# Optimization experiments

Hardware: AMD Instinct MI355X
Metric: run time of the kernel (lower is better)

## Reference

```python
import jax, jax.numpy as jnp
import numpy as np

FFT_LENGTH = 2048
HOP_LENGTH = 512  # window_length // 4, window_length == fft_length


def _hann_periodic(n):
    # tf.signal.hann_window(n, periodic=True)
    return (0.5 - 0.5 * jnp.cos(2.0 * jnp.pi * jnp.arange(n) / n)).astype(jnp.float32)


def setup_inputs() -> dict:
    key = jax.random.key(0)
    k1, k2 = jax.random.split(key)
    B, F, NB = 4, 4000, FFT_LENGTH // 2 + 1
    spec_real = jax.random.normal(k1, (B, F, NB), dtype=jnp.float32)
    spec_imag = jax.random.normal(k2, (B, F, NB), dtype=jnp.float32)
    return {"spec_real": spec_real, "spec_imag": spec_imag}


def reference(spec_real, spec_imag) -> jnp.ndarray:
    fft_length, hop = FFT_LENGTH, HOP_LENGTH
    B, F, _ = spec_real.shape
    window = _hann_periodic(fft_length)  # [N], window_length == fft_length so no padding

    # irfft of the complex spectrogram -> time-domain frames [B, F, N]
    frames = jnp.fft.irfft(spec_real + 1j * spec_imag, n=fft_length).astype(jnp.float32)
    windowed = window * frames  # [B, F, N]

    # overlap-and-add: output length L = (F-1)*hop + N
    L = (F - 1) * hop + fft_length
    idx = (jnp.arange(F) * hop)[:, None] + jnp.arange(fft_length)[None, :]  # [F, N]
    out = jnp.zeros((B, L), jnp.float32).at[:, idx].add(windowed)

    # librosa window_sumsquare: overlap-add of squared window, guard tiny values
    wsq = jnp.zeros((L,), jnp.float32).at[idx].add(window * window)
    tiny = jnp.float32(np.finfo(np.float32).tiny)
    window_sum = jnp.where(wsq > tiny, wsq, jnp.float32(1.0))

    y = out / window_sum
    # center=True: trim fft_length//2 on each side
    half = fft_length // 2
    return y[:, half:L - half]
```

## Files before the change

kernel.cpp:

```cpp
#include <hip/hip_runtime.h>
#include <math.h>

#define NB       1025
#define M        1024
#define FFTN     2048
#define HOP      512
#define NFRAMES  4000
#define BATCH    4
#define OUT_T    2047488
#define R_HOPS   8
#define REG_PB   501
#define PI_F     3.14159265358979323846f

__device__ __forceinline__ float2 cmul(float2 a, float2 b) {
    return make_float2(a.x*b.x - a.y*b.y, a.x*b.y + a.y*b.x);
}
__device__ __forceinline__ int SW(int i) { return i ^ ((i >> 4) & 15); }

__device__ __forceinline__ float wsq_at(int p) {
    int u  = p + FFTN / 2;
    int fm = u >> 9;
    int n0 = u & 511;
    float wsq = 0.f;
    #pragma unroll
    for (int jj = 0; jj < 4; ++jj) {
        int fr = fm - jj;
        if (fr >= 0 && fr < NFRAMES) {
            int n = n0 + (jj << 9);
            float sw = __sinf((PI_F / (float)FFTN) * (float)n);
            float w  = sw * sw;
            wsq += w * w;
        }
    }
    const float tiny = 1.17549435e-38f;
    return (wsq > tiny) ? wsq : 1.0f;
}

__device__ __forceinline__ float invw_at(int p, bool edge) {
    if (edge && (p < 512 || p >= OUT_T - 512)) return 1.0f / wsq_at(p);
    return (2.0f / 3.0f);
}

template<int ST>
__device__ __forceinline__ void stage(const float2* __restrict__ src,
                                      float2* __restrict__ dst, int j, float2 w1) {
    const int Ns = 1 << (2 * ST);
    float2 v0 = src[SW(j)];
    float2 v1 = src[SW(j + 256)];
    float2 v2 = src[SW(j + 512)];
    float2 v3 = src[SW(j + 768)];
    float2 w2 = cmul(w1, w1);
    float2 w3 = cmul(w2, w1);
    v1 = cmul(v1, w1); v2 = cmul(v2, w2); v3 = cmul(v3, w3);
    float2 t0 = make_float2(v0.x + v2.x, v0.y + v2.y);
    float2 t1 = make_float2(v0.x - v2.x, v0.y - v2.y);
    float2 t2 = make_float2(v1.x + v3.x, v1.y + v3.y);
    float2 t3 = make_float2(v1.x - v3.x, v1.y - v3.y);
    int jm = j & (Ns - 1);
    int idxD = ((j >> (2 * ST)) << (2 * ST + 2)) + jm;
    dst[SW(idxD         )] = make_float2(t0.x + t2.x, t0.y + t2.y);
    dst[SW(idxD +     Ns)] = make_float2(t1.x - t3.y, t1.y + t3.x);
    dst[SW(idxD + 2 * Ns)] = make_float2(t0.x - t2.x, t0.y - t2.y);
    dst[SW(idxD + 3 * Ns)] = make_float2(t1.x + t3.y, t1.y - t3.x);
}

__device__ __forceinline__ void pack_st0(float2* __restrict__ dst, int j,
                                         const float2* tw_pack,
                                         const float* car, const float* cai,
                                         const float* cbr, const float* cbi) {
    float2 z[4];
    #pragma unroll
    for (int kk = 0; kk < 4; ++kk) {
        float arv = car[kk], aiv = cai[kk];
        float brv = cbr[kk], biv = cbi[kk];
        if (kk == 0 && j == 0) { aiv = 0.f; biv = 0.f; }
        float Er = 0.5f * (arv + brv), Ei = 0.5f * (aiv - biv);
        float Dr = 0.5f * (arv - brv), Di = 0.5f * (aiv + biv);
        float2 t = tw_pack[kk];
        float Or = Dr * t.x - Di * t.y;
        float Oi = Dr * t.y + Di * t.x;
        z[kk] = make_float2(Er - Oi, Ei + Or);
    }
    float2 t0 = make_float2(z[0].x + z[2].x, z[0].y + z[2].y);
    float2 t1 = make_float2(z[0].x - z[2].x, z[0].y - z[2].y);
    float2 t2 = make_float2(z[1].x + z[3].x, z[1].y + z[3].y);
    float2 t3 = make_float2(z[1].x - z[3].x, z[1].y - z[3].y);
    dst[SW(4*j    )] = make_float2(t0.x + t2.x, t0.y + t2.y);
    dst[SW(4*j + 1)] = make_float2(t1.x - t3.y, t1.y + t3.x);
    dst[SW(4*j + 2)] = make_float2(t0.x - t2.x, t0.y - t2.y);
    dst[SW(4*j + 3)] = make_float2(t1.x + t3.y, t1.y - t3.x);
}

__device__ __forceinline__ void load_spec(const float* __restrict__ sr,
                                          const float* __restrict__ si,
                                          int b, int f, int j,
                                          float* car, float* cai,
                                          float* cbr, float* cbi) {
    const size_t fb = ((size_t)b * NFRAMES + f) * NB;
    const float* __restrict__ xr = sr + fb;
    const float* __restrict__ xi = si + fb;
    #pragma unroll
    for (int kk = 0; kk < 4; ++kk) {
        int k  = j + kk * 256;
        int mk = M - k;
        car[kk] = xr[k];  cai[kk] = xi[k];
        cbr[kk] = xr[mk]; cbi[kk] = xi[mk];
    }
}

__global__ __launch_bounds__(256) void istft_regacc_kernel(
    const float* __restrict__ sr, const float* __restrict__ si,
    float* __restrict__ out)
{
    __shared__ float2 buf0[M];
    __shared__ float2 buf1[M];

    const int blk = blockIdx.x;
    const int b   = blk / REG_PB;
    const int reg = blk - b * REG_PB;
    const int s0h = reg * R_HOPS;
    const int j   = threadIdx.x;
    const bool edge = (reg == 0) || (reg == REG_PB - 1);

    float2 tw_pack[4];
    #pragma unroll
    for (int kk = 0; kk < 4; ++kk) {
        int k = j + kk * 256;
        float s, c;
        __sincosf(PI_F * (float)k * (1.0f / (float)M), &s, &c);
        tw_pack[kk] = make_float2(c, s);
    }
    float2 w1s[4];
    #pragma unroll
    for (int st = 1; st <= 4; ++st) {
        int Ns = 1 << (2 * st);
        int jm = j & (Ns - 1);
        float ang = (0.5f * PI_F / (float)Ns) * (float)jm;
        float s1, c1;
        __sincosf(ang, &s1, &c1);
        w1s[st-1] = make_float2(c1, s1);
    }
    float wreg[4][2];
    #pragma unroll
    for (int q = 0; q < 4; ++q) {
        int n = j + q * 256;
        #pragma unroll
        for (int h = 0; h < 2; ++h) {
            int t = 2 * n + h;
            float swv = __sinf((PI_F / (float)FFTN) * (float)t);
            wreg[q][h] = swv * swv * (1.0f / 1024.0f);
        }
    }

    float2 A[R_HOPS];
    #pragma unroll
    for (int s = 0; s < R_HOPS; ++s) A[s] = make_float2(0.f, 0.f);

    const int fbase = s0h - 3;

    float car[4], cai[4], cbr[4], cbi[4];
    {
        int it0 = (fbase < 0) ? -fbase : 0;
        int ff  = fbase + it0;
        if (ff > NFRAMES - 1) ff = NFRAMES - 1;
        load_spec(sr, si, b, ff, j, car, cai, cbr, cbi);
    }

    #pragma unroll
    for (int it = 0; it < 11; ++it) {
        const int f = fbase + it;
        const bool valid = (f >= 0) && (f < NFRAMES);
        if (valid) {
            pack_st0(buf0, j, tw_pack, car, cai, cbr, cbi);

            float nar[4], nai[4], nbr[4], nbi[4];
            const int fn = f + 1;
            const bool nvalid = (it < 10) && (fn < NFRAMES);
            if (nvalid) load_spec(sr, si, b, fn, j, nar, nai, nbr, nbi);

            __syncthreads();
            stage<1>(buf0, buf1, j, w1s[0]);
            __syncthreads();
            stage<2>(buf1, buf0, j, w1s[1]);
            __syncthreads();
            stage<3>(buf0, buf1, j, w1s[2]);
            __syncthreads();

            {
                float2 v0 = buf1[SW(j)];
                float2 v1 = buf1[SW(j + 256)];
                float2 v2 = buf1[SW(j + 512)];
                float2 v3 = buf1[SW(j + 768)];
                float2 w1 = w1s[3];
                float2 w2 = cmul(w1, w1);
                float2 w3 = cmul(w2, w1);
                v1 = cmul(v1, w1); v2 = cmul(v2, w2); v3 = cmul(v3, w3);
                float2 t0 = make_float2(v0.x + v2.x, v0.y + v2.y);
                float2 t1 = make_float2(v0.x - v2.x, v0.y - v2.y);
                float2 t2 = make_float2(v1.x + v3.x, v1.y + v3.y);
                float2 t3 = make_float2(v1.x - v3.x, v1.y - v3.y);
                float2 g[4];
                g[0] = make_float2(t0.x + t2.x, t0.y + t2.y);
                g[1] = make_float2(t1.x - t3.y, t1.y + t3.x);
                g[2] = make_float2(t0.x - t2.x, t0.y - t2.y);
                g[3] = make_float2(t1.x + t3.y, t1.y - t3.x);
                #pragma unroll
                for (int q = 0; q < 4; ++q) {
                    const int s = it - 3 + q;
                    if (s >= 0 && s < R_HOPS) {
                        A[s].x += g[q].x * wreg[q][0];
                        A[s].y += g[q].y * wreg[q][1];
                    }
                }
            }

            if (nvalid) {
                #pragma unroll
                for (int kk = 0; kk < 4; ++kk) {
                    car[kk] = nar[kk]; cai[kk] = nai[kk];
                    cbr[kk] = nbr[kk]; cbi[kk] = nbi[kk];
                }
            }
        }
    }

    const int base_u = s0h * HOP;
    float* outb = out + (size_t)b * OUT_T;
    #pragma unroll
    for (int s = 0; s < R_HOPS; ++s) {
        int i2 = j + 256 * s;
        int p0 = base_u + 2 * i2 - FFTN / 2;
        int p1 = p0 + 1;
        if ((unsigned)p0 < (unsigned)OUT_T) outb[p0] = A[s].x * invw_at(p0, edge);
        if ((unsigned)p1 < (unsigned)OUT_T) outb[p1] = A[s].y * invw_at(p1, edge);
    }
}

extern "C" void kernel_launch(void* const* d_in, const int* in_sizes, int n_in,
                              void* d_out, int out_size, void* d_ws, size_t ws_size,
                              hipStream_t stream) {
    const float* sr = (const float*)d_in[0];
    const float* si = (const float*)d_in[1];
    float* out = (float*)d_out;
    istft_regacc_kernel<<<BATCH * REG_PB, 256, 0, stream>>>(sr, si, out);
}
```

Baseline: 56.88 us.

## Process two overlap-add regions per block with float4-packed FFT stages

Each block now computes two adjacent output regions, running two frames' inverse FFTs at once by packing them into float4 shared-memory elements. This halves the block count and amortizes barriers and twiddle math across two transforms. The next-frame register prefetch is dropped, so loads are no longer overlapped with compute, and shared memory use and register pressure both double.

```diff
diff --git a/kernel.cpp b/kernel.cpp
--- a/kernel.cpp
+++ b/kernel.cpp
@@ -9,13 +9,22 @@
 #define BATCH    4
 #define OUT_T    2047488
 #define R_HOPS   8
-#define REG_PB   501
+#define NPAIR    251
 #define PI_F     3.14159265358979323846f
 
 __device__ __forceinline__ float2 cmul(float2 a, float2 b) {
     return make_float2(a.x*b.x - a.y*b.y, a.x*b.y + a.y*b.x);
 }
-__device__ __forceinline__ int SW(int i) { return i ^ ((i >> 4) & 15); }
+__device__ __forceinline__ float4 cmul4(float4 v, float2 w) {
+    return make_float4(v.x*w.x - v.y*w.y, v.x*w.y + v.y*w.x,
+                       v.z*w.x - v.w*w.y, v.z*w.y + v.w*w.x);
+}
+__device__ __forceinline__ float4 f4add(float4 a, float4 b){ return make_float4(a.x+b.x, a.y+b.y, a.z+b.z, a.w+b.w); }
+__device__ __forceinline__ float4 f4sub(float4 a, float4 b){ return make_float4(a.x-b.x, a.y-b.y, a.z-b.z, a.w-b.w); }
+__device__ __forceinline__ float4 f4addi(float4 a, float4 b){ return make_float4(a.x-b.y, a.y+b.x, a.z-b.w, a.w+b.z); }
+__device__ __forceinline__ float4 f4subi(float4 a, float4 b){ return make_float4(a.x+b.y, a.y-b.x, a.z+b.w, a.w-b.z); }
+
+__device__ __forceinline__ int SW4(int i) { return i ^ ((i >> 3) & 7); }
 
 __device__ __forceinline__ float wsq_at(int p) {
     int u  = p + FFTN / 2;
@@ -35,60 +44,30 @@
     const float tiny = 1.17549435e-38f;
     return (wsq > tiny) ? wsq : 1.0f;
 }
-
 __device__ __forceinline__ float invw_at(int p, bool edge) {
     if (edge && (p < 512 || p >= OUT_T - 512)) return 1.0f / wsq_at(p);
     return (2.0f / 3.0f);
 }
 
 template<int ST>
-__device__ __forceinline__ void stage(const float2* __restrict__ src,
-                                      float2* __restrict__ dst, int j, float2 w1) {
+__device__ __forceinline__ void stage4x(const float4* __restrict__ src,
+                                        float4* __restrict__ dst, int j, float2 w1) {
     const int Ns = 1 << (2 * ST);
-    float2 v0 = src[SW(j)];
-    float2 v1 = src[SW(j + 256)];
-    float2 v2 = src[SW(j + 512)];
-    float2 v3 = src[SW(j + 768)];
+    float4 v0 = src[SW4(j)];
+    float4 v1 = src[SW4(j + 256)];
+    float4 v2 = src[SW4(j + 512)];
+    float4 v3 = src[SW4(j + 768)];
     float2 w2 = cmul(w1, w1);
     float2 w3 = cmul(w2, w1);
-    v1 = cmul(v1, w1); v2 = cmul(v2, w2); v3 = cmul(v3, w3);
-    float2 t0 = make_float2(v0.x + v2.x, v0.y + v2.y);
-    float2 t1 = make_float2(v0.x - v2.x, v0.y - v2.y);
-    float2 t2 = make_float2(v1.x + v3.x, v1.y + v3.y);
-    float2 t3 = make_float2(v1.x - v3.x, v1.y - v3.y);
+    v1 = cmul4(v1, w1); v2 = cmul4(v2, w2); v3 = cmul4(v3, w3);
+    float4 t0 = f4add(v0, v2), t1 = f4sub(v0, v2);
+    float4 t2 = f4add(v1, v3), t3 = f4sub(v1, v3);
     int jm = j & (Ns - 1);
     int idxD = ((j >> (2 * ST)) << (2 * ST + 2)) + jm;
-    dst[SW(idxD         )] = make_float2(t0.x + t2.x, t0.y + t2.y);
-    dst[SW(idxD +     Ns)] = make_float2(t1.x - t3.y, t1.y + t3.x);
-    dst[SW(idxD + 2 * Ns)] = make_float2(t0.x - t2.x, t0.y - t2.y);
-    dst[SW(idxD + 3 * Ns)] = make_float2(t1.x + t3.y, t1.y - t3.x);
-}
-
-__device__ __forceinline__ void pack_st0(float2* __restrict__ dst, int j,
-                                         const float2* tw_pack,
-                                         const float* car, const float* cai,
-                                         const float* cbr, const float* cbi) {
-    float2 z[4];
-    #pragma unroll
-    for (int kk = 0; kk < 4; ++kk) {
-        float arv = car[kk], aiv = cai[kk];
-        float brv = cbr[kk], biv = cbi[kk];
-        if (kk == 0 && j == 0) { aiv = 0.f; biv = 0.f; }
-        float Er = 0.5f * (arv + brv), Ei = 0.5f * (aiv - biv);
-        float Dr = 0.5f * (arv - brv), Di = 0.5f * (aiv + biv);
-        float2 t = tw_pack[kk];
-        float Or = Dr * t.x - Di * t.y;
-        float Oi = Dr * t.y + Di * t.x;
-        z[kk] = make_float2(Er - Oi, Ei + Or);
-    }
-    float2 t0 = make_float2(z[0].x + z[2].x, z[0].y + z[2].y);
-    float2 t1 = make_float2(z[0].x - z[2].x, z[0].y - z[2].y);
-    float2 t2 = make_float2(z[1].x + z[3].x, z[1].y + z[3].y);
-    float2 t3 = make_float2(z[1].x - z[3].x, z[1].y - z[3].y);
-    dst[SW(4*j    )] = make_float2(t0.x + t2.x, t0.y + t2.y);
-    dst[SW(4*j + 1)] = make_float2(t1.x - t3.y, t1.y + t3.x);
-    dst[SW(4*j + 2)] = make_float2(t0.x - t2.x, t0.y - t2.y);
-    dst[SW(4*j + 3)] = make_float2(t1.x + t3.y, t1.y - t3.x);
+    dst[SW4(idxD         )] = f4add(t0, t2);
+    dst[SW4(idxD +     Ns)] = f4addi(t1, t3);
+    dst[SW4(idxD + 2 * Ns)] = f4sub(t0, t2);
+    dst[SW4(idxD + 3 * Ns)] = f4subi(t1, t3);
 }
 
 __device__ __forceinline__ void load_spec(const float* __restrict__ sr,
@@ -108,19 +87,49 @@
     }
 }
 
-__global__ __launch_bounds__(256) void istft_regacc_kernel(
+__device__ __forceinline__ void pack2_st0(float4* __restrict__ dst, int j,
+                                          const float2* twp,
+                                          const float* a1r, const float* a1i,
+                                          const float* b1r, const float* b1i,
+                                          const float* a2r, const float* a2i,
+                                          const float* b2r, const float* b2i) {
+    float4 z[4];
+    #pragma unroll
+    for (int kk = 0; kk < 4; ++kk) {
+        float ar = a1r[kk], ai = a1i[kk], br = b1r[kk], bi = b1i[kk];
+        float cr = a2r[kk], ci = a2i[kk], dr = b2r[kk], di = b2i[kk];
+        if (kk == 0 && j == 0) { ai = 0.f; bi = 0.f; ci = 0.f; di = 0.f; }
+        float2 t = twp[kk];
+        float Er = 0.5f*(ar+br), Ei = 0.5f*(ai-bi), Dr = 0.5f*(ar-br), Di = 0.5f*(ai+bi);
+        float Or = Dr*t.x - Di*t.y, Oi = Dr*t.y + Di*t.x;
+        float Fr = 0.5f*(cr+dr), Fi = 0.5f*(ci-di), Gr = 0.5f*(cr-dr), Gi = 0.5f*(ci+di);
+        float Pr = Gr*t.x - Gi*t.y, Pi = Gr*t.y + Gi*t.x;
+        z[kk] = make_float4(Er - Oi, Ei + Or, Fr - Pi, Fi + Pr);
+    }
+    float4 t0 = f4add(z[0], z[2]), t1 = f4sub(z[0], z[2]);
+    float4 t2 = f4add(z[1], z[3]), t3 = f4sub(z[1], z[3]);
+    dst[SW4(4*j    )] = f4add(t0, t2);
+    dst[SW4(4*j + 1)] = f4addi(t1, t3);
+    dst[SW4(4*j + 2)] = f4sub(t0, t2);
+    dst[SW4(4*j + 3)] = f4subi(t1, t3);
+}
+
+__global__ __launch_bounds__(256) void istft_pair_kernel(
     const float* __restrict__ sr, const float* __restrict__ si,
     float* __restrict__ out)
 {
-    __shared__ float2 buf0[M];
-    __shared__ float2 buf1[M];
-
-    const int blk = blockIdx.x;
-    const int b   = blk / REG_PB;
-    const int reg = blk - b * REG_PB;
-    const int s0h = reg * R_HOPS;
-    const int j   = threadIdx.x;
-    const bool edge = (reg == 0) || (reg == REG_PB - 1);
+    __shared__ float4 buf0[M];
+    __shared__ float4 buf1[M];
+
+    const int blk  = blockIdx.x;
+    const int b    = blk / NPAIR;
+    const int pr   = blk - b * NPAIR;
+    const int regA = 2 * pr;
+    const int s0hA = regA * R_HOPS;
+    const int s0hB = s0hA + R_HOPS;
+    const int j    = threadIdx.x;
+    const bool edgeA = (regA == 0) || (regA == 500);
+    const bool edgeB = (regA + 1 == 500);
 
     float2 tw_pack[4];
     #pragma unroll
@@ -152,87 +161,100 @@
         }
     }
 
-    float2 A[R_HOPS];
-    #pragma unroll
-    for (int s = 0; s < R_HOPS; ++s) A[s] = make_float2(0.f, 0.f);
-
-    const int fbase = s0h - 3;
-
-    float car[4], cai[4], cbr[4], cbi[4];
-    {
-        int it0 = (fbase < 0) ? -fbase : 0;
-        int ff  = fbase + it0;
-        if (ff > NFRAMES - 1) ff = NFRAMES - 1;
-        load_spec(sr, si, b, ff, j, car, cai, cbr, cbi);
+    float2 AccA[R_HOPS], AccB[R_HOPS];
+    #pragma unroll
+    for (int s = 0; s < R_HOPS; ++s) {
+        AccA[s] = make_float2(0.f, 0.f);
+        AccB[s] = make_float2(0.f, 0.f);
     }
 
     #pragma unroll
     for (int it = 0; it < 11; ++it) {
-        const int f = fbase + it;
-        const bool valid = (f >= 0) && (f < NFRAMES);
-        if (valid) {
-            pack_st0(buf0, j, tw_pack, car, cai, cbr, cbi);
-
-            float nar[4], nai[4], nbr[4], nbi[4];
-            const int fn = f + 1;
-            const bool nvalid = (it < 10) && (fn < NFRAMES);
-            if (nvalid) load_spec(sr, si, b, fn, j, nar, nai, nbr, nbi);
-
-            __syncthreads();
-            stage<1>(buf0, buf1, j, w1s[0]);
-            __syncthreads();
-            stage<2>(buf1, buf0, j, w1s[1]);
-            __syncthreads();
-            stage<3>(buf0, buf1, j, w1s[2]);
-            __syncthreads();
-
-            {
-                float2 v0 = buf1[SW(j)];
-                float2 v1 = buf1[SW(j + 256)];
-                float2 v2 = buf1[SW(j + 512)];
-                float2 v3 = buf1[SW(j + 768)];
-                float2 w1 = w1s[3];
-                float2 w2 = cmul(w1, w1);
-                float2 w3 = cmul(w2, w1);
-                v1 = cmul(v1, w1); v2 = cmul(v2, w2); v3 = cmul(v3, w3);
-                float2 t0 = make_float2(v0.x + v2.x, v0.y + v2.y);
-                float2 t1 = make_float2(v0.x - v2.x, v0.y - v2.y);
-                float2 t2 = make_float2(v1.x + v3.x, v1.y + v3.y);
-                float2 t3 = make_float2(v1.x - v3.x, v1.y - v3.y);
-                float2 g[4];
-                g[0] = make_float2(t0.x + t2.x, t0.y + t2.y);
-                g[1] = make_float2(t1.x - t3.y, t1.y + t3.x);
-                g[2] = make_float2(t0.x - t2.x, t0.y - t2.y);
-                g[3] = make_float2(t1.x + t3.y, t1.y - t3.x);
+        const int fA = s0hA - 3 + it;
+        const int fB = s0hB - 3 + it;
+        const bool vA = (fA >= 0) && (fA < NFRAMES);
+        const bool vB = (fB >= 0) && (fB < NFRAMES);
+        if (!vA && !vB) continue;
+
+        int fAc = fA < 0 ? 0 : (fA > NFRAMES-1 ? NFRAMES-1 : fA);
+        int fBc = fB < 0 ? 0 : (fB > NFRAMES-1 ? NFRAMES-1 : fB);
+
+        float a1r[4], a1i[4], b1r[4], b1i[4];
+        float a2r[4], a2i[4], b2r[4], b2i[4];
+        load_spec(sr, si, b, fAc, j, a1r, a1i, b1r, b1i);
+        load_spec(sr, si, b, fBc, j, a2r, a2i, b2r, b2i);
+
+        pack2_st0(buf0, j, tw_pack, a1r, a1i, b1r, b1i, a2r, a2i, b2r, b2i);
+        __syncthreads();
+        stage4x<1>(buf0, buf1, j, w1s[0]);
+        __syncthreads();
+        stage4x<2>(buf1, buf0, j, w1s[1]);
+        __syncthreads();
+        stage4x<3>(buf0, buf1, j, w1s[2]);
+        __syncthreads();
+
+        {
+            float4 v0 = buf1[SW4(j)];
+            float4 v1 = buf1[SW4(j + 256)];
+            float4 v2 = buf1[SW4(j + 512)];
+            float4 v3 = buf1[SW4(j + 768)];
+            float2 w1 = w1s[3];
+            float2 w2 = cmul(w1, w1);
+            float2 w3 = cmul(w2, w1);
+            v1 = cmul4(v1, w1); v2 = cmul4(v2, w2); v3 = cmul4(v3, w3);
+            float4 t0 = f4add(v0, v2), t1 = f4sub(v0, v2);
+            float4 t2 = f4add(v1, v3), t3 = f4sub(v1, v3);
+            float4 g[4];
+            g[0] = f4add(t0, t2);
+            g[1] = f4addi(t1, t3);
+            g[2] = f4sub(t0, t2);
+            g[3] = f4subi(t1, t3);
+            if (vA) {
                 #pragma unroll
                 for (int q = 0; q < 4; ++q) {
                     const int s = it - 3 + q;
                     if (s >= 0 && s < R_HOPS) {
-                        A[s].x += g[q].x * wreg[q][0];
-                        A[s].y += g[q].y * wreg[q][1];
+                        AccA[s].x += g[q].x * wreg[q][0];
+                        AccA[s].y += g[q].y * wreg[q][1];
                     }
                 }
             }
-
-            if (nvalid) {
+            if (vB) {
                 #pragma unroll
-                for (int kk = 0; kk < 4; ++kk) {
-                    car[kk] = nar[kk]; cai[kk] = nai[kk];
-                    cbr[kk] = nbr[kk]; cbi[kk] = nbi[kk];
+                for (int q = 0; q < 4; ++q) {
+                    const int s = it - 3 + q;
+                    if (s >= 0 && s < R_HOPS) {
+                        AccB[s].x += g[q].z * wreg[q][0];
+                        AccB[s].y += g[q].w * wreg[q][1];
+                    }
                 }
             }
         }
-    }
-
-    const int base_u = s0h * HOP;
+        __syncthreads();
+    }
+
     float* outb = out + (size_t)b * OUT_T;
-    #pragma unroll
-    for (int s = 0; s < R_HOPS; ++s) {
-        int i2 = j + 256 * s;
-        int p0 = base_u + 2 * i2 - FFTN / 2;
-        int p1 = p0 + 1;
-        if ((unsigned)p0 < (unsigned)OUT_T) outb[p0] = A[s].x * invw_at(p0, edge);
-        if ((unsigned)p1 < (unsigned)OUT_T) outb[p1] = A[s].y * invw_at(p1, edge);
+    {
+        const int base_u = s0hA * HOP;
+        #pragma unroll
+        for (int s = 0; s < R_HOPS; ++s) {
+            int i2 = j + 256 * s;
+            int p0 = base_u + 2 * i2 - FFTN / 2;
+            int p1 = p0 + 1;
+            if ((unsigned)p0 < (unsigned)OUT_T) outb[p0] = AccA[s].x * invw_at(p0, edgeA);
+            if ((unsigned)p1 < (unsigned)OUT_T) outb[p1] = AccA[s].y * invw_at(p1, edgeA);
+        }
+    }
+    {
+        const int base_u = s0hB * HOP;
+        #pragma unroll
+        for (int s = 0; s < R_HOPS; ++s) {
+            int i2 = j + 256 * s;
+            int p0 = base_u + 2 * i2 - FFTN / 2;
+            int p1 = p0 + 1;
+            if ((unsigned)p0 < (unsigned)OUT_T) outb[p0] = AccB[s].x * invw_at(p0, edgeB);
+            if ((unsigned)p1 < (unsigned)OUT_T) outb[p1] = AccB[s].y * invw_at(p1, edgeB);
+        }
     }
 }
 
@@ -242,5 +264,5 @@
     const float* sr = (const float*)d_in[0];
     const float* si = (const float*)d_in[1];
     float* out = (float*)d_out;
-    istft_regacc_kernel<<<BATCH * REG_PB, 256, 0, stream>>>(sr, si, out);
-}
+    istft_pair_kernel<<<BATCH * NPAIR, 256, 0, stream>>>(sr, si, out);
+}
```

Measured after the change: 53.92 us. -5.2%, faster.
